# Kernel optimization log

Hardware: AMD Instinct MI355X
Metric: run time of the kernel (lower is better)

The kernel has to match this reference:

```python
import jax, jax.numpy as jnp
import numpy as np

NUM_HEADS = 16

def setup_inputs() -> dict:
    key = jax.random.key(0)
    k1, k2, k3 = jax.random.split(key, 3)
    B, T, D = 4, 2048, 1024
    x = jax.random.normal(k1, (B, T, D), dtype=jnp.float32)
    # lecun_normal: std = 1/sqrt(fan_in)
    w = jax.random.normal(k2, (3 * D, D), dtype=jnp.float32) * (1.0 / np.sqrt(D))
    w_out = jax.random.normal(k3, (D, D), dtype=jnp.float32) * (1.0 / np.sqrt(D))
    return {"x": x, "w": w, "w_out": w_out}


def reference(x, w, w_out):
    B, T, D = x.shape
    H = NUM_HEADS
    L = D // H
    # qkv projection: (B,T,3D)
    q, k, v = jnp.split(jnp.matmul(x, w.T), 3, axis=2)
    # -> (T,B,H,L) time-major for the scan
    q = q.reshape(B, T, H, L).transpose(1, 0, 2, 3)
    k = k.reshape(B, T, H, L).transpose(1, 0, 2, 3)
    v = v.reshape(B, T, H, L).transpose(1, 0, 2, 3)
    scale = jax.lax.rsqrt(jnp.float32(L))
    k_exp = jnp.exp(k * scale) + 1e-6            # (T,B,H,L)
    k_norm = jnp.cumsum(k_exp, axis=0)           # causal normalizer
    qs = jax.nn.softmax(q * scale, axis=-1) / k_norm

    def step(carry, args):
        qs_t, k_t, v_t = args                    # each (B,H,L)
        # accumulate outer product k_t v_t^T into (B,H,L,L) state
        carry = carry + k_t[..., :, None] * v_t[..., None, :]
        y_t = jnp.einsum('bhl,bhlm->bhm', qs_t, carry)
        return carry, y_t

    init = jnp.zeros((B, H, L, L), dtype=x.dtype)
    _, y = jax.lax.scan(step, init, (qs, k_exp, v))   # y: (T,B,H,L)
    y = y.reshape(T, B, D).transpose(1, 0, 2)         # (B,T,D)
    return jnp.matmul(y, w_out)                       # Dense, no bias
```

## Files before the change

### kernel.cpp

```cpp
#include <hip/hip_runtime.h>
#include <math.h>

#define Bsz   4
#define Tsz   2048
#define Dsz   1024
#define Hsz   16
#define Lsz   64
#define BHsz  64
#define CH    64
#define NCH   32
#define QKVLD 3072
#define SCL   0.125f
#define QSC   512.0f
#define QSCI  (1.0f/512.0f)

typedef float  floatx4 __attribute__((ext_vector_type(4)));
typedef _Float16 half8 __attribute__((ext_vector_type(8)));
typedef _Float16 half4 __attribute__((ext_vector_type(4)));
typedef _Float16 half2v __attribute__((ext_vector_type(2)));

#define AS1 __attribute__((address_space(1)))
#define AS3 __attribute__((address_space(3)))

static __device__ __forceinline__ void gload_lds16(const void* g, void* l) {
  __builtin_amdgcn_global_load_lds((const AS1 unsigned int*)g,
                                   (AS3 unsigned int*)l, 16, 0, 0);
}

static __device__ __forceinline__ float wave_max64(float v) {
#pragma unroll
  for (int off = 1; off < 64; off <<= 1) v = fmaxf(v, __shfl_xor(v, off));
  return v;
}
static __device__ __forceinline__ float wave_sum64(float v) {
#pragma unroll
  for (int off = 1; off < 64; off <<= 1) v += __shfl_xor(v, off);
  return v;
}

__launch_bounds__(256)
__global__ void prep(const float* __restrict__ x, _Float16* __restrict__ xh,
                     const float* __restrict__ w, _Float16* __restrict__ wh,
                     const float* __restrict__ wo, _Float16* __restrict__ woT) {
  const int blk = blockIdx.x, tid = threadIdx.x;
  if (blk < 11264) {
    const float* in  = (blk < 8192) ? x : w;
    _Float16*   outp = (blk < 8192) ? xh : wh;
    const int bi = (blk < 8192) ? blk : blk - 8192;
    const int i = (bi * 256 + tid) * 4;
    float4 v = *(const float4*)(in + i);
    half4 h = { (_Float16)v.x, (_Float16)v.y, (_Float16)v.z, (_Float16)v.w };
    *(half4*)(outp + i) = h;
  } else {
    __shared__ float tile[32][33];
    const int bi = blk - 11264;
    const int bx = (bi & 31) * 32;
    const int by = (bi >> 5) * 32;
    const int tx = tid & 31, ty0 = tid >> 5;
#pragma unroll
    for (int p = 0; p < 4; p++) {
      const int ty = ty0 + p * 8;
      tile[ty][tx] = wo[(size_t)(by + ty) * 1024 + bx + tx];
    }
    __syncthreads();
#pragma unroll
    for (int p = 0; p < 4; p++) {
      const int ty = ty0 + p * 8;
      woT[(size_t)(bx + ty) * 1024 + by + tx] = (_Float16)tile[tx][ty];
    }
  }
}

__launch_bounds__(256)
__global__ void gemm_f16_bt_f32(const _Float16* __restrict__ A, const _Float16* __restrict__ B,
                                float* __restrict__ C, int M, int N, int K) {
  __shared__ _Float16 As[128][32];
  __shared__ _Float16 Bs[128][32];
  const int tid  = threadIdx.x;
  const int wave = tid >> 6, lane = tid & 63;
  const int m0 = blockIdx.y * 128, n0 = blockIdx.x * 128;
  const int wm = (wave >> 1) * 64, wn = (wave & 1) * 64;
  const int fr = lane & 15;
  const int fq = lane >> 4;
  const int lr = lane >> 2;
  const int lk = (lane & 3) * 8;

  floatx4 zero = {0.f, 0.f, 0.f, 0.f};
  floatx4 acc[4][4];
#pragma unroll
  for (int mt = 0; mt < 4; mt++)
#pragma unroll
    for (int nt = 0; nt < 4; nt++) acc[mt][nt] = zero;

  for (int k0 = 0; k0 < K; k0 += 32) {
    __syncthreads();
#pragma unroll
    for (int j = 0; j < 2; j++) {
      const int ia = wave * 2 + j;
      gload_lds16(A + (size_t)(m0 + ia * 16 + lr) * K + k0 + lk, &As[ia * 16][0]);
      gload_lds16(B + (size_t)(n0 + ia * 16 + lr) * K + k0 + lk, &Bs[ia * 16][0]);
    }
    __syncthreads();

    half8 af[4], bf[4];
#pragma unroll
    for (int i = 0; i < 4; i++) {
      af[i] = *(const half8*)&As[wm + i * 16 + fr][fq * 8];
      bf[i] = *(const half8*)&Bs[wn + i * 16 + fr][fq * 8];
    }
#pragma unroll
    for (int mt = 0; mt < 4; mt++)
#pragma unroll
      for (int nt = 0; nt < 4; nt++)
        acc[mt][nt] = __builtin_amdgcn_mfma_f32_16x16x32_f16(af[mt], bf[nt], acc[mt][nt], 0, 0, 0);
  }
#pragma unroll
  for (int mt = 0; mt < 4; mt++)
#pragma unroll
    for (int nt = 0; nt < 4; nt++)
#pragma unroll
      for (int r = 0; r < 4; r++) {
        const int row = m0 + wm + mt * 16 + fq * 4 + r;
        const int col = n0 + wn + nt * 16 + fr;
        C[(size_t)row * N + col] = acc[mt][nt][r];
      }
}

__launch_bounds__(256)
__global__ void gemm_f16_bt_c16(const _Float16* __restrict__ A, const _Float16* __restrict__ B,
                                _Float16* __restrict__ C, int M, int N, int K) {
  __shared__ _Float16 As[128][32];
  __shared__ _Float16 Bs[128][32];
  const int tid  = threadIdx.x;
  const int wave = tid >> 6, lane = tid & 63;
  const int m0 = blockIdx.y * 128, n0 = blockIdx.x * 128;
  const int wm = (wave >> 1) * 64, wn = (wave & 1) * 64;
  const int fr = lane & 15;
  const int fq = lane >> 4;
  const int lr = lane >> 2;
  const int lk = (lane & 3) * 8;
  const bool kreg = (n0 >= 1024) && (n0 < 2048);

  floatx4 zero = {0.f, 0.f, 0.f, 0.f};
  floatx4 acc[4][4];
#pragma unroll
  for (int mt = 0; mt < 4; mt++)
#pragma unroll
    for (int nt = 0; nt < 4; nt++) acc[mt][nt] = zero;

  for (int k0 = 0; k0 < K; k0 += 32) {
    __syncthreads();
#pragma unroll
    for (int j = 0; j < 2; j++) {
      const int ia = wave * 2 + j;
      gload_lds16(A + (size_t)(m0 + ia * 16 + lr) * K + k0 + lk, &As[ia * 16][0]);
      gload_lds16(B + (size_t)(n0 + ia * 16 + lr) * K + k0 + lk, &Bs[ia * 16][0]);
    }
    __syncthreads();

    half8 af[4], bf[4];
#pragma unroll
    for (int i = 0; i < 4; i++) {
      af[i] = *(const half8*)&As[wm + i * 16 + fr][fq * 8];
      bf[i] = *(const half8*)&Bs[wn + i * 16 + fr][fq * 8];
    }
#pragma unroll
    for (int mt = 0; mt < 4; mt++)
#pragma unroll
      for (int nt = 0; nt < 4; nt++)
        acc[mt][nt] = __builtin_amdgcn_mfma_f32_16x16x32_f16(af[mt], bf[nt], acc[mt][nt], 0, 0, 0);
  }
#pragma unroll
  for (int mt = 0; mt < 4; mt++)
#pragma unroll
    for (int nt = 0; nt < 4; nt++)
#pragma unroll
      for (int r = 0; r < 4; r++) {
        const int row = m0 + wm + mt * 16 + fq * 4 + r;
        const int col = n0 + wn + nt * 16 + fr;
        float v = acc[mt][nt][r];
        if (kreg) v = __expf(v * SCL) + 1e-6f;
        C[(size_t)row * N + col] = (_Float16)v;
      }
}

__launch_bounds__(256)
__global__ void chunk_kv(const _Float16* __restrict__ qkv, float* __restrict__ KV,
                         float* __restrict__ Ksum) {
  const int blk = blockIdx.x;
  const int bh = blk >> 3, cgrp = blk & 7;
  const int b = bh >> 4, h = bh & 15;
  const int tid = threadIdx.x;
  const int wave = tid >> 6, lane = tid & 63;
  const int fr = lane & 15, fq = lane >> 4;
  const int m2  = (tid & 31) * 2;
  const int tg8 = (tid >> 5) * 8;

  __shared__ __align__(16) _Float16 KxT[64][72];
  __shared__ __align__(16) _Float16 VT [64][72];

  for (int cc = 0; cc < 4; cc++) {
    const int c = cgrp * 4 + cc;
    const size_t base = ((size_t)(b * Tsz + c * CH)) * QKVLD + h * 64;
    __syncthreads();
    half8 klo, khi, vlo, vhi;
#pragma unroll
    for (int j = 0; j < 8; j++) {
      const int t = tg8 + j;
      half2v kk = *(const half2v*)(qkv + base + (size_t)t * QKVLD + 1024 + m2);
      klo[j] = kk[0]; khi[j] = kk[1];
      half2v vv = *(const half2v*)(qkv + base + (size_t)t * QKVLD + 2048 + m2);
      vlo[j] = vv[0]; vhi[j] = vv[1];
    }
    *(half8*)&KxT[m2][tg8]     = klo;
    *(half8*)&KxT[m2 + 1][tg8] = khi;
    *(half8*)&VT[m2][tg8]      = vlo;
    *(half8*)&VT[m2 + 1][tg8]  = vhi;
    __syncthreads();

    floatx4 acc[4];
#pragma unroll
    for (int j = 0; j < 4; j++) acc[j] = (floatx4){0.f, 0.f, 0.f, 0.f};
#pragma unroll
    for (int ks = 0; ks < 2; ks++) {
      half8 av = *(const half8*)&VT[wave * 16 + fr][ks * 32 + fq * 8];
#pragma unroll
      for (int j = 0; j < 4; j++) {
        half8 bv = *(const half8*)&KxT[j * 16 + fr][ks * 32 + fq * 8];
        acc[j] = __builtin_amdgcn_mfma_f32_16x16x32_f16(av, bv, acc[j], 0, 0, 0);
      }
    }
    float* KVp = KV + ((size_t)(bh * NCH + c)) * 4096;
#pragma unroll
    for (int j = 0; j < 4; j++)
#pragma unroll
      for (int r = 0; r < 4; r++)
        KVp[(wave * 16 + fq * 4 + r) * 64 + j * 16 + fr] = acc[j][r];

    if (tid < 64) {
      float s = 0.f;
      const half8* row = (const half8*)&KxT[tid][0];
#pragma unroll
      for (int j8 = 0; j8 < 8; j8++) {
        half8 v8 = row[j8];
#pragma unroll
        for (int j = 0; j < 8; j++) s += (float)v8[j];
      }
      Ksum[(bh * NCH + c) * 64 + tid] = s;
    }
  }
}

__launch_bounds__(256)
__global__ void prefix_kern(float* __restrict__ KV, float* __restrict__ Ksum) {
  const int tid = threadIdx.x;
  if (blockIdx.x < 1024) {
    const int bh = blockIdx.x >> 4;
    const int e  = (blockIdx.x & 15) * 256 + tid;
    float* p = KV + (size_t)bh * NCH * 4096 + e;
    float acc = 0.f;
#pragma unroll 4
    for (int c = 0; c < NCH; c++) {
      float t = p[(size_t)c * 4096];
      p[(size_t)c * 4096] = acc;
      acc += t;
    }
  } else {
    const int cid = (blockIdx.x - 1024) * 256 + tid;
    const int bh = cid >> 6, l = cid & 63;
    float* p = Ksum + bh * NCH * 64 + l;
    float acc = 0.f;
#pragma unroll 4
    for (int c = 0; c < NCH; c++) {
      float t = p[c * 64];
      p[c * 64] = acc;
      acc += t;
    }
  }
}

__launch_bounds__(256)
__global__ void chunk_y(const _Float16* __restrict__ qkv, const float* __restrict__ KV,
                        const float* __restrict__ Ksum, _Float16* __restrict__ Y) {
  const int bh = blockIdx.x, c = blockIdx.y;
  const int b = bh >> 4, h = bh & 15;
  const int tid = threadIdx.x;
  const int wave = tid >> 6, lane = tid & 63;
  const int fr = lane & 15, fq = lane >> 4;

  __shared__ __align__(16) _Float16 kxh[64][72];
  __shared__ __align__(16) _Float16 kxT[64][72];
  __shared__ __align__(16) _Float16 Ph[64][136];
  __shared__ __align__(16) _Float16 Bh[64][136];

  const size_t base = ((size_t)(b * Tsz + c * CH)) * QKVLD + h * 64;
  const float* KVp = KV + ((size_t)(bh * NCH + c)) * 4096;
  const int ksoff = (bh * NCH + c) * 64;

  _Float16 qreg[16];
#pragma unroll
  for (int i = 0; i < 16; i++)
    qreg[i] = qkv[base + (size_t)(wave * 16 + i) * QKVLD + lane];

  float ksb[4];
#pragma unroll
  for (int j = 0; j < 4; j++) ksb[j] = Ksum[ksoff + j * 16 + fr];

  {
    const int rr  = tid >> 3;
    const int sg8 = (tid & 7) * 8;
#pragma unroll
    for (int p = 0; p < 2; p++) {
      const int t = p * 32 + rr;
      *(half8*)&kxh[t][sg8] =
          *(const half8*)(qkv + base + (size_t)t * QKVLD + 1024 + sg8);
    }
  }
  {
    const int m2  = (tid & 31) * 2;
    const int tg8 = (tid >> 5) * 8;
    half8 klo, khi, vlo, vhi;
#pragma unroll
    for (int j = 0; j < 8; j++) {
      const int t = tg8 + j;
      half2v kk = *(const half2v*)(qkv + base + (size_t)t * QKVLD + 1024 + m2);
      klo[j] = kk[0]; khi[j] = kk[1];
      half2v vv = *(const half2v*)(qkv + base + (size_t)t * QKVLD + 2048 + m2);
      vlo[j] = vv[0]; vhi[j] = vv[1];
    }
    *(half8*)&kxT[m2][tg8]         = klo;
    *(half8*)&kxT[m2 + 1][tg8]     = khi;
    *(half8*)&Bh[m2][64 + tg8]     = vlo;
    *(half8*)&Bh[m2 + 1][64 + tg8] = vhi;
  }
  {
    const int m  = tid >> 2;
    const int l0 = (tid & 3) * 16;
#pragma unroll
    for (int q = 0; q < 2; q++) {
      float4 s0 = *(const float4*)(KVp + m * 64 + l0 + q * 8);
      float4 s1 = *(const float4*)(KVp + m * 64 + l0 + q * 8 + 4);
      half8 hh = { (_Float16)s0.x, (_Float16)s0.y, (_Float16)s0.z, (_Float16)s0.w,
                   (_Float16)s1.x, (_Float16)s1.y, (_Float16)s1.z, (_Float16)s1.w };
      *(half8*)&Bh[m][l0 + q * 8] = hh;
    }
  }
  __syncthreads();

  {
    floatx4 kacc[4];
#pragma unroll
    for (int j = 0; j < 4; j++) kacc[j] = (floatx4){0.f, 0.f, 0.f, 0.f};
#pragma unroll
    for (int ks = 0; ks < 2; ks++) {
      half8 af;
#pragma unroll
      for (int j = 0; j < 8; j++)
        af[j] = (ks * 32 + fq * 8 + j) <= (wave * 16 + fr) ? (_Float16)1.0f
                                                           : (_Float16)0.0f;
#pragma unroll
      for (int j = 0; j < 4; j++) {
        half8 bf = *(const half8*)&kxT[j * 16 + fr][ks * 32 + fq * 8];
        kacc[j] = __builtin_amdgcn_mfma_f32_16x16x32_f16(af, bf, kacc[j], 0, 0, 0);
      }
    }
    __syncthreads();
#pragma unroll
    for (int j = 0; j < 4; j++)
#pragma unroll
      for (int r = 0; r < 4; r++)
        kxT[wave * 16 + fq * 4 + r][j * 16 + fr] =
            (_Float16)(QSC / (ksb[j] + kacc[j][r]));
  }

#pragma unroll
  for (int i = 0; i < 16; i++) {
    const int t = wave * 16 + i;
    float v = (float)qreg[i] * SCL;
    float m = wave_max64(v);
    float e = __expf(v - m);
    float s = wave_sum64(e);
    Ph[t][lane] = (_Float16)((e / s) * (float)kxT[t][lane]);
  }
  __syncthreads();

  const int wm = (wave >> 1) * 32, wn = (wave & 1) * 32;
  {
    floatx4 a2[2][2];
#pragma unroll
    for (int mt = 0; mt < 2; mt++)
#pragma unroll
      for (int nt = 0; nt < 2; nt++) a2[mt][nt] = (floatx4){0.f, 0.f, 0.f, 0.f};
#pragma unroll
    for (int ks = 0; ks < 2; ks++) {
      half8 af[2], bf[2];
#pragma unroll
      for (int i = 0; i < 2; i++) {
        af[i] = *(const half8*)&Ph[wm + i * 16 + fr][ks * 32 + fq * 8];
        bf[i] = *(const half8*)&kxh[wn + i * 16 + fr][ks * 32 + fq * 8];
      }
#pragma unroll
      for (int mt = 0; mt < 2; mt++)
#pragma unroll
        for (int nt = 0; nt < 2; nt++)
          a2[mt][nt] = __builtin_amdgcn_mfma_f32_16x16x32_f16(af[mt], bf[nt], a2[mt][nt], 0, 0, 0);
    }
#pragma unroll
    for (int mt = 0; mt < 2; mt++)
#pragma unroll
      for (int nt = 0; nt < 2; nt++)
#pragma unroll
        for (int r = 0; r < 4; r++) {
          const int t = wm + mt * 16 + fq * 4 + r;
          const int s = wn + nt * 16 + fr;
          Ph[t][64 + s] = (_Float16)(s <= t ? a2[mt][nt][r] : 0.f);
        }
  }
  __syncthreads();

  {
    floatx4 acc[2][2];
#pragma unroll
    for (int mt = 0; mt < 2; mt++)
#pragma unroll
      for (int nt = 0; nt < 2; nt++) acc[mt][nt] = (floatx4){0.f, 0.f, 0.f, 0.f};
#pragma unroll
    for (int ks = 0; ks < 4; ks++) {
      half8 af[2], bf[2];
#pragma unroll
      for (int i = 0; i < 2; i++) {
        af[i] = *(const half8*)&Ph[wm + i * 16 + fr][ks * 32 + fq * 8];
        bf[i] = *(const half8*)&Bh[wn + i * 16 + fr][ks * 32 + fq * 8];
      }
#pragma unroll
      for (int mt = 0; mt < 2; mt++)
#pragma unroll
        for (int nt = 0; nt < 2; nt++)
          acc[mt][nt] = __builtin_amdgcn_mfma_f32_16x16x32_f16(af[mt], bf[nt], acc[mt][nt], 0, 0, 0);
    }
#pragma unroll
    for (int mt = 0; mt < 2; mt++)
#pragma unroll
      for (int nt = 0; nt < 2; nt++)
#pragma unroll
        for (int r = 0; r < 4; r++)
          kxh[wm + mt * 16 + fq * 4 + r][wn + nt * 16 + fr] =
              (_Float16)(acc[mt][nt][r] * QSCI);
  }
  __syncthreads();

  {
    const int ty = tid >> 2, sg = (tid & 3) * 16;
    _Float16* yrow = Y + (size_t)(b * Tsz + c * CH + ty) * Dsz + h * 64 + sg;
    *(half8*)(yrow)     = *(const half8*)&kxh[ty][sg];
    *(half8*)(yrow + 8) = *(const half8*)&kxh[ty][sg + 8];
  }
}

extern "C" void kernel_launch(void* const* d_in, const int* in_sizes, int n_in,
                              void* d_out, int out_size, void* d_ws, size_t ws_size,
                              hipStream_t stream) {
  const float* x     = (const float*)d_in[0];
  const float* w     = (const float*)d_in[1];
  const float* w_out = (const float*)d_in[2];
  float* out = (float*)d_out;

  _Float16* xh   = (_Float16*)d_ws;
  _Float16* Yh   = xh;
  _Float16* wh   = xh + (size_t)8192 * 1024;
  _Float16* woT  = wh + (size_t)3072 * 1024;
  _Float16* qkvh = woT + (size_t)1024 * 1024;
  float* KV   = (float*)(qkvh + (size_t)8192 * 3072);
  float* Ksum = KV + (size_t)BHsz * NCH * 4096;

  prep<<<12288, 256, 0, stream>>>(x, xh, w, wh, w_out, woT);

  gemm_f16_bt_c16<<<dim3(24, 64), 256, 0, stream>>>(xh, wh, qkvh, 8192, 3072, 1024);

  chunk_kv<<<512, 256, 0, stream>>>(qkvh, KV, Ksum);
  prefix_kern<<<1040, 256, 0, stream>>>(KV, Ksum);
  chunk_y<<<dim3(BHsz, NCH), 256, 0, stream>>>(qkvh, KV, Ksum, Yh);

  gemm_f16_bt_f32<<<dim3(8, 64), 256, 0, stream>>>(Yh, woT, out, 8192, 1024, 1024);
}
```

Before: 257.8 us.

## Remap GEMM tiles per XCD, vectorize prefix scan, stage K/V transposes via LDS

Both GEMMs now remap the flat block index so that consecutive blocks on the same XCD (flat & 7) share M-row tiles, which should improve L2 reuse of A-tiles on the multi-die MI355X. The prefix scan kernel now processes float4 per thread with a quarter as many blocks, giving wider coalesced loads and stores. In chunk_y the strided half2 global gathers for the K/V transposes are replaced by coalesced half8 global loads into LDS, with the transpose done from LDS, at the cost of an extra barrier. Ph is reused as scratch for V before it is overwritten later.

```diff
diff --git a/kernel.cpp b/kernel.cpp
--- a/kernel.cpp
+++ b/kernel.cpp
@@ -78,7 +78,10 @@
   __shared__ _Float16 Bs[128][32];
   const int tid  = threadIdx.x;
   const int wave = tid >> 6, lane = tid & 63;
-  const int m0 = blockIdx.y * 128, n0 = blockIdx.x * 128;
+  const int flat = blockIdx.y * gridDim.x + blockIdx.x;
+  const int xcd = flat & 7, g = flat >> 3;
+  const int m0 = (xcd * 8 + (g & 7)) * 128;
+  const int n0 = (g >> 3) * 128;
   const int wm = (wave >> 1) * 64, wn = (wave & 1) * 64;
   const int fr = lane & 15;
   const int fq = lane >> 4;
@@ -133,7 +136,10 @@
   __shared__ _Float16 Bs[128][32];
   const int tid  = threadIdx.x;
   const int wave = tid >> 6, lane = tid & 63;
-  const int m0 = blockIdx.y * 128, n0 = blockIdx.x * 128;
+  const int flat = blockIdx.y * gridDim.x + blockIdx.x;
+  const int xcd = flat & 7, g = flat >> 3;
+  const int m0 = (xcd * 8 + (g & 7)) * 128;
+  const int n0 = (g >> 3) * 128;
   const int wm = (wave >> 1) * 64, wn = (wave & 1) * 64;
   const int fr = lane & 15;
   const int fq = lane >> 4;
@@ -254,27 +260,27 @@
 __launch_bounds__(256)
 __global__ void prefix_kern(float* __restrict__ KV, float* __restrict__ Ksum) {
   const int tid = threadIdx.x;
-  if (blockIdx.x < 1024) {
-    const int bh = blockIdx.x >> 4;
-    const int e  = (blockIdx.x & 15) * 256 + tid;
-    float* p = KV + (size_t)bh * NCH * 4096 + e;
-    float acc = 0.f;
+  if (blockIdx.x < 256) {
+    const int bh = blockIdx.x >> 2;
+    const int e  = (blockIdx.x & 3) * 1024 + tid * 4;
+    float4* p = (float4*)(KV + (size_t)bh * NCH * 4096 + e);
+    float4 acc = {0.f, 0.f, 0.f, 0.f};
 #pragma unroll 4
     for (int c = 0; c < NCH; c++) {
-      float t = p[(size_t)c * 4096];
-      p[(size_t)c * 4096] = acc;
-      acc += t;
+      float4 t = p[(size_t)c * 1024];
+      p[(size_t)c * 1024] = acc;
+      acc.x += t.x; acc.y += t.y; acc.z += t.z; acc.w += t.w;
     }
   } else {
-    const int cid = (blockIdx.x - 1024) * 256 + tid;
-    const int bh = cid >> 6, l = cid & 63;
-    float* p = Ksum + bh * NCH * 64 + l;
-    float acc = 0.f;
+    const int cid = (blockIdx.x - 256) * 256 + tid;
+    const int bh = cid >> 4, l4 = cid & 15;
+    float4* p = (float4*)(Ksum + (size_t)bh * NCH * 64) + l4;
+    float4 acc = {0.f, 0.f, 0.f, 0.f};
 #pragma unroll 4
     for (int c = 0; c < NCH; c++) {
-      float t = p[c * 64];
-      p[c * 64] = acc;
-      acc += t;
+      float4 t = p[c * 16];
+      p[c * 16] = acc;
+      acc.x += t.x; acc.y += t.y; acc.z += t.z; acc.w += t.w;
     }
   }
 }
@@ -314,24 +320,9 @@
       const int t = p * 32 + rr;
       *(half8*)&kxh[t][sg8] =
           *(const half8*)(qkv + base + (size_t)t * QKVLD + 1024 + sg8);
-    }
-  }
-  {
-    const int m2  = (tid & 31) * 2;
-    const int tg8 = (tid >> 5) * 8;
-    half8 klo, khi, vlo, vhi;
-#pragma unroll
-    for (int j = 0; j < 8; j++) {
-      const int t = tg8 + j;
-      half2v kk = *(const half2v*)(qkv + base + (size_t)t * QKVLD + 1024 + m2);
-      klo[j] = kk[0]; khi[j] = kk[1];
-      half2v vv = *(const half2v*)(qkv + base + (size_t)t * QKVLD + 2048 + m2);
-      vlo[j] = vv[0]; vhi[j] = vv[1];
-    }
-    *(half8*)&kxT[m2][tg8]         = klo;
-    *(half8*)&kxT[m2 + 1][tg8]     = khi;
-    *(half8*)&Bh[m2][64 + tg8]     = vlo;
-    *(half8*)&Bh[m2 + 1][64 + tg8] = vhi;
+      *(half8*)&Ph[t][64 + sg8] =
+          *(const half8*)(qkv + base + (size_t)t * QKVLD + 2048 + sg8);
+    }
   }
   {
     const int m  = tid >> 2;
@@ -344,6 +335,25 @@
                    (_Float16)s1.x, (_Float16)s1.y, (_Float16)s1.z, (_Float16)s1.w };
       *(half8*)&Bh[m][l0 + q * 8] = hh;
     }
+  }
+  __syncthreads();
+
+  {
+    const int l2  = (tid & 31) * 2;
+    const int tg8 = (tid >> 5) * 8;
+    half8 k0, k1, v0, v1;
+#pragma unroll
+    for (int j = 0; j < 8; j++) {
+      const int t = tg8 + j;
+      half2v kk = *(const half2v*)&kxh[t][l2];
+      k0[j] = kk[0]; k1[j] = kk[1];
+      half2v vv = *(const half2v*)&Ph[t][64 + l2];
+      v0[j] = vv[0]; v1[j] = vv[1];
+    }
+    *(half8*)&kxT[l2][tg8]          = k0;
+    *(half8*)&kxT[l2 + 1][tg8]      = k1;
+    *(half8*)&Bh[l2][64 + tg8]      = v0;
+    *(half8*)&Bh[l2 + 1][64 + tg8]  = v1;
   }
   __syncthreads();
 
@@ -478,7 +488,7 @@
   gemm_f16_bt_c16<<<dim3(24, 64), 256, 0, stream>>>(xh, wh, qkvh, 8192, 3072, 1024);
 
   chunk_kv<<<512, 256, 0, stream>>>(qkvh, KV, Ksum);
-  prefix_kern<<<1040, 256, 0, stream>>>(KV, Ksum);
+  prefix_kern<<<260, 256, 0, stream>>>(KV, Ksum);
   chunk_y<<<dim3(BHsz, NCH), 256, 0, stream>>>(qkvh, KV, Ksum, Yh);
 
   gemm_f16_bt_f32<<<dim3(8, 64), 256, 0, stream>>>(Yh, woT, out, 8192, 1024, 1024);
```

After: 249.4 us. 1.03x faster.
